# Performance work log

Hardware: AMD Instinct MI355X
Metric: run time of the kernel (lower is better)

## Reference

```python
import jax, jax.numpy as jnp
import numpy as np

B, S, D = 2, 2048, 1024
H_Q, H_KV, DK, DV = 16, 8, 64, 64
R = H_Q // H_KV  # q heads per kv head (GQA)
THETA = 10000.0


def setup_inputs() -> dict:
    key = jax.random.key(0)
    ks = jax.random.split(key, 12)
    inv_freq = 1.0 / (THETA ** (jnp.arange(0, DK, 2, dtype=jnp.float32) / DK))  # [DK/2]
    angles = jnp.arange(S, dtype=jnp.float32)[:, None] * inv_freq[None, :]      # [S, DK/2]
    scale = 0.02
    return {
        "x": jax.random.normal(ks[0], (B, S, D), jnp.float32),
        "Wq": jax.random.normal(ks[1], (D, H_Q * DK), jnp.float32) * scale,
        "bq": jnp.zeros((H_Q * DK,), jnp.float32),
        "Wk": jax.random.normal(ks[2], (D, H_KV * DK), jnp.float32) * scale,
        "bk": jnp.zeros((H_KV * DK,), jnp.float32),
        "Wv": jax.random.normal(ks[3], (D, H_KV * DV), jnp.float32) * scale,
        "bv": jnp.zeros((H_KV * DV,), jnp.float32),
        "Wo": jax.random.normal(ks[4], (H_Q * DV, D), jnp.float32) * scale,
        "bo": jnp.zeros((D,), jnp.float32),
        "freqs_cos": jnp.cos(angles),
        "freqs_sin": jnp.sin(angles),
        "attention_mask": jax.random.bernoulli(ks[5], 0.9, (B, S)),  # True = real token
    }


def _rope(t, cos, sin):
    # t: [B, S, H, Dh]; cos/sin: [S, Dh/2]. Complex rotation on interleaved pairs.
    tp = t.reshape(*t.shape[:-1], -1, 2)
    x1, x2 = tp[..., 0], tp[..., 1]
    c = cos[None, :, None, :]
    s = sin[None, :, None, :]
    o1 = x1 * c - x2 * s
    o2 = x1 * s + x2 * c
    return jnp.stack([o1, o2], axis=-1).reshape(t.shape)


def reference(x, Wq, bq, Wk, bk, Wv, bv, Wo, bo, freqs_cos, freqs_sin, attention_mask):
    b, s, _ = x.shape
    q = (x @ Wq + bq).reshape(b, s, H_Q, DK)
    k = (x @ Wk + bk).reshape(b, s, H_KV, DK)
    v = (x @ Wv + bv).reshape(b, s, H_KV, DV)
    q = _rope(q, freqs_cos, freqs_sin)
    k = _rope(k, freqs_cos, freqs_sin)
    q = q.transpose(0, 2, 1, 3)                      # [B, Hq, S, DK]
    k = jnp.repeat(k.transpose(0, 2, 1, 3), R, axis=1)  # GQA expand -> [B, Hq, S, DK]
    v = jnp.repeat(v.transpose(0, 2, 1, 3), R, axis=1)  # [B, Hq, S, DV]
    causal = jnp.tril(jnp.ones((s, s), dtype=bool))
    # Module does logical_or(padding, causal) -- replicated faithfully.
    mask = jnp.logical_or(attention_mask[:, None, None, :], causal[None, None])
    scale = 1.0 / jnp.sqrt(jnp.float32(DK))
    scores = jnp.einsum('bhqd,bhkd->bhqk', q, k) * scale
    scores = jnp.where(mask, scores, -jnp.inf)
    attn = jax.nn.softmax(scores, axis=-1)
    out = jnp.einsum('bhqk,bhkd->bhqd', attn, v)
    out = out.transpose(0, 2, 1, 3).reshape(b, s, H_Q * DV)
    return out @ Wo + bo
```

## Files before the change

kernel.cpp:

```cpp
#include <hip/hip_runtime.h>
#include <hip/hip_bf16.h>
#include <math.h>

typedef __attribute__((ext_vector_type(8))) short bf16x8;
typedef __attribute__((ext_vector_type(4))) float f32x4;

#define OFF_XB  0ull
#define OFF_WT  (8ull<<20)
#define OFF_WO  (12ull<<20)
#define OFF_QB  (14ull<<20)
#define OFF_KB  (22ull<<20)
#define OFF_VT  (26ull<<20)
#define OFF_AO  (30ull<<20)
#define OFF_MB  (38ull<<20)

#define QSCALE 0.18033688056680276f

__device__ inline unsigned pack_bf162(float a, float b) {
    __hip_bfloat162 t = __float22bfloat162_rn(make_float2(a, b));
    return *(unsigned*)&t;
}

__device__ inline float exp2_fast(float x) {
    float r;
    asm("v_exp_f32 %0, %1" : "=v"(r) : "v"(x));
    return r;
}

__device__ inline void gload16(const void* g, void* l) {
    __builtin_amdgcn_global_load_lds(
        (const __attribute__((address_space(1))) void*)g,
        (__attribute__((address_space(3))) void*)l, 16, 0, 0);
}

__launch_bounds__(256)
__global__ void prep_kernel(const float* __restrict__ x,
                            const float* __restrict__ Wq, const float* __restrict__ Wk,
                            const float* __restrict__ Wv, const float* __restrict__ Wo,
                            const void* __restrict__ mraw,
                            __hip_bfloat16* __restrict__ XB,
                            __hip_bfloat16* __restrict__ WT,
                            __hip_bfloat16* __restrict__ WoT,
                            float* __restrict__ mbias) {
    __shared__ float T[32][33];
    __shared__ int bad01, badf;
    const int tid = threadIdx.x;
    const int bid = blockIdx.x;
    if (bid < 1024) {
        const int base = bid * 4096;
#pragma unroll
        for (int i = 0; i < 4; ++i) {
            const int e = base + (i * 256 + tid) * 4;
            const float4 v = *(const float4*)&x[e];
            uint2 pk;
            pk.x = pack_bf162(v.x, v.y);
            pk.y = pack_bf162(v.z, v.w);
            *(uint2*)&XB[e] = pk;
        }
    } else if (bid < 4096) {
        const float* src; int ldn, nbase; __hip_bfloat16* dst; int n0, k0;
        if (bid < 3072) {
            const int tb = bid - 1024;
            const int kt = tb >> 6, nt = tb & 63;
            n0 = nt * 32; k0 = kt * 32; dst = WT;
            if (n0 < 1024)      { src = Wq; ldn = 1024; nbase = n0; }
            else if (n0 < 1536) { src = Wk; ldn = 512;  nbase = n0 - 1024; }
            else                { src = Wv; ldn = 512;  nbase = n0 - 1536; }
        } else {
            const int tb = bid - 3072;
            const int kt = tb >> 5, nt = tb & 31;
            n0 = nt * 32; k0 = kt * 32; dst = WoT;
            src = Wo; ldn = 1024; nbase = n0;
        }
        const int c = tid & 31, r0 = tid >> 5;
#pragma unroll
        for (int i = 0; i < 4; ++i)
            T[r0 + 8 * i][c] = src[(size_t)(k0 + r0 + 8 * i) * ldn + nbase + c];
        __syncthreads();
#pragma unroll
        for (int i = 0; i < 4; ++i) {
            const int nn = r0 + 8 * i;
            dst[(size_t)(n0 + nn) * 1024 + k0 + c] = __float2bfloat16(T[c][nn]);
        }
    } else {
        if (tid == 0) { bad01 = 0; badf = 0; }
        __syncthreads();
        const unsigned* w = (const unsigned*)mraw;
#pragma unroll
        for (int i = 0; i < 4; ++i) {
            const unsigned v = w[tid * 4 + i];
            if (v > 1u) atomicAdd(&bad01, 1);
            if (v != 0u && v != 0x3F800000u) atomicAdd(&badf, 1);
        }
        __syncthreads();
        const int fmt = (bad01 == 0) ? 0 : ((badf == 0) ? 1 : 2);
        for (int i = tid; i < 4096; i += 256) {
            bool on;
            if (fmt == 2) on = (((const unsigned char*)mraw)[i] != 0);
            else          on = (w[i] != 0u);
            mbias[i] = on ? 0.f : -1e30f;
        }
    }
}

#define QSTAGE(SEL, K0_) do {                                                    \
    _Pragma("unroll") for (int rnd_ = 0; rnd_ < 4; ++rnd_) {                     \
        const int off_ = rnd_ * 4096 + wid * 1024 + lane * 16;                   \
        const int row_ = off_ >> 7;                                              \
        const int ch_  = ((off_ >> 4) & 7) ^ (row_ & 7);                         \
        gload16((const char*)Ag + ((size_t)(n0 + row_) * 1024 + (K0_) + ch_ * 8) * 2, \
                Asm + (SEL) * 16384 + rnd_ * 4096 + wid * 1024);                 \
        gload16((const char*)Bg + ((size_t)(m0 + row_) * 1024 + (K0_) + ch_ * 8) * 2, \
                Bsm + (SEL) * 16384 + rnd_ * 4096 + wid * 1024);                 \
    }                                                                            \
} while (0)

__launch_bounds__(256)
__global__ void qkv_mfma_kernel(const __hip_bfloat16* __restrict__ XB,
                                const __hip_bfloat16* __restrict__ WT,
                                const float* __restrict__ bq, const float* __restrict__ bk,
                                const float* __restrict__ bv,
                                const float* __restrict__ fc, const float* __restrict__ fs,
                                __hip_bfloat16* __restrict__ QB,
                                __hip_bfloat16* __restrict__ KB,
                                __hip_bfloat16* __restrict__ VT) {
    __shared__ __attribute__((aligned(16))) char Asm[32768];
    __shared__ __attribute__((aligned(16))) char Bsm[32768];
    const int tid = threadIdx.x;
    const int lane = tid & 63, wid = tid >> 6;
    const int c = lane & 15, g = lane >> 4;
    const int n0 = blockIdx.x * 128, m0 = blockIdx.y * 128;
    const int wn = (wid >> 1) * 64, wm = (wid & 1) * 64;
    const __hip_bfloat16* Ag = WT;
    const __hip_bfloat16* Bg = XB;

    f32x4 acc[4][4];
#pragma unroll
    for (int ni = 0; ni < 4; ++ni)
#pragma unroll
        for (int mj = 0; mj < 4; ++mj) acc[ni][mj] = f32x4{0.f, 0.f, 0.f, 0.f};

    QSTAGE(0, 0);
    int cur = 0;
    for (int kt = 0; kt < 16; ++kt) {
        const int k0 = kt * 64;
        if (kt < 15) {
            QSTAGE(cur ^ 1, k0 + 64);
            asm volatile("s_waitcnt vmcnt(8)" ::: "memory");
        } else {
            asm volatile("s_waitcnt vmcnt(0)" ::: "memory");
        }
        __builtin_amdgcn_sched_barrier(0);
        __builtin_amdgcn_s_barrier();
        __builtin_amdgcn_sched_barrier(0);

        const char* Ac = Asm + cur * 16384;
        const char* Bc = Bsm + cur * 16384;
#pragma unroll
        for (int ks = 0; ks < 2; ++ks) {
            bf16x8 af[4], bfr[4];
#pragma unroll
            for (int t = 0; t < 4; ++t) {
                const int sl = ((g + 4 * ks) ^ (c & 7)) << 4;
                af[t]  = *(const bf16x8*)(Ac + (wn + 16 * t + c) * 128 + sl);
                bfr[t] = *(const bf16x8*)(Bc + (wm + 16 * t + c) * 128 + sl);
            }
#pragma unroll
            for (int ni = 0; ni < 4; ++ni)
#pragma unroll
                for (int mj = 0; mj < 4; ++mj)
                    acc[ni][mj] = __builtin_amdgcn_mfma_f32_16x16x32_bf16(
                        af[ni], bfr[mj], acc[ni][mj], 0, 0, 0);
        }
        __builtin_amdgcn_sched_barrier(0);
        __builtin_amdgcn_s_barrier();
        __builtin_amdgcn_sched_barrier(0);
        cur ^= 1;
    }

#pragma unroll
    for (int ni = 0; ni < 4; ++ni) {
        const int nb = n0 + wn + 16 * ni + 4 * g;
        const float* bias; int nloc;
        if (nb < 1024)      { bias = bq; nloc = nb; }
        else if (nb < 1536) { bias = bk; nloc = nb - 1024; }
        else                { bias = bv; nloc = nb - 1536; }
        const float4 b4 = *(const float4*)&bias[nloc];
        const int h = nloc >> 6, dk = nb & 63;
#pragma unroll
        for (int mj = 0; mj < 4; ++mj) {
            const int tok = m0 + wm + 16 * mj + c;
            const int bb = tok >> 11, sp = tok & 2047;
            float v0 = acc[ni][mj][0] + b4.x;
            float v1 = acc[ni][mj][1] + b4.y;
            float v2 = acc[ni][mj][2] + b4.z;
            float v3 = acc[ni][mj][3] + b4.w;
            if (nb < 1536) {
                const int p = sp * 32 + (dk >> 1);
                const float c0 = fc[p], s0 = fs[p];
                const float c1 = fc[p + 1], s1 = fs[p + 1];
                float o0 = v0 * c0 - v1 * s0, o1 = v0 * s0 + v1 * c0;
                float o2 = v2 * c1 - v3 * s1, o3 = v2 * s1 + v3 * c1;
                uint2 pk;
                if (nb < 1024) {
                    o0 *= QSCALE; o1 *= QSCALE; o2 *= QSCALE; o3 *= QSCALE;
                    pk.x = pack_bf162(o0, o1); pk.y = pack_bf162(o2, o3);
                    *(uint2*)&QB[(size_t)((bb * 16 + h) * 2048 + sp) * 64 + dk] = pk;
                } else {
                    pk.x = pack_bf162(o0, o1); pk.y = pack_bf162(o2, o3);
                    *(uint2*)&KB[(size_t)((bb * 8 + h) * 2048 + sp) * 64 + dk] = pk;
                }
            } else {
                const size_t vb = (size_t)((bb * 8 + h) * 64 + dk) * 2048 + sp;
                VT[vb]          = __float2bfloat16(v0);
                VT[vb + 2048]   = __float2bfloat16(v1);
                VT[vb + 4096]   = __float2bfloat16(v2);
                VT[vb + 6144]   = __float2bfloat16(v3);
            }
        }
    }
}

__launch_bounds__(256)
__global__ void out_mfma_kernel(const __hip_bfloat16* __restrict__ AOB,
                                const __hip_bfloat16* __restrict__ WoT,
                                const float* __restrict__ bo,
                                float* __restrict__ out) {
    __shared__ __attribute__((aligned(16))) char Asm[32768];
    __shared__ __attribute__((aligned(16))) char Bsm[32768];
    const int tid = threadIdx.x;
    const int lane = tid & 63, wid = tid >> 6;
    const int c = lane & 15, g = lane >> 4;
    const int n0 = blockIdx.x * 128, m0 = blockIdx.y * 128;
    const int wn = (wid >> 1) * 64, wm = (wid & 1) * 64;
    const __hip_bfloat16* Ag = WoT;
    const __hip_bfloat16* Bg = AOB;

    f32x4 acc[4][4];
#pragma unroll
    for (int ni = 0; ni < 4; ++ni)
#pragma unroll
        for (int mj = 0; mj < 4; ++mj) acc[ni][mj] = f32x4{0.f, 0.f, 0.f, 0.f};

    QSTAGE(0, 0);
    int cur = 0;
    for (int kt = 0; kt < 16; ++kt) {
        const int k0 = kt * 64;
        if (kt < 15) {
            QSTAGE(cur ^ 1, k0 + 64);
            asm volatile("s_waitcnt vmcnt(8)" ::: "memory");
        } else {
            asm volatile("s_waitcnt vmcnt(0)" ::: "memory");
        }
        __builtin_amdgcn_sched_barrier(0);
        __builtin_amdgcn_s_barrier();
        __builtin_amdgcn_sched_barrier(0);

        const char* Ac = Asm + cur * 16384;
        const char* Bc = Bsm + cur * 16384;
#pragma unroll
        for (int ks = 0; ks < 2; ++ks) {
            bf16x8 af[4], bfr[4];
#pragma unroll
            for (int t = 0; t < 4; ++t) {
                const int sl = ((g + 4 * ks) ^ (c & 7)) << 4;
                af[t]  = *(const bf16x8*)(Ac + (wn + 16 * t + c) * 128 + sl);
                bfr[t] = *(const bf16x8*)(Bc + (wm + 16 * t + c) * 128 + sl);
            }
#pragma unroll
            for (int ni = 0; ni < 4; ++ni)
#pragma unroll
                for (int mj = 0; mj < 4; ++mj)
                    acc[ni][mj] = __builtin_amdgcn_mfma_f32_16x16x32_bf16(
                        af[ni], bfr[mj], acc[ni][mj], 0, 0, 0);
        }
        __builtin_amdgcn_sched_barrier(0);
        __builtin_amdgcn_s_barrier();
        __builtin_amdgcn_sched_barrier(0);
        cur ^= 1;
    }
#pragma unroll
    for (int ni = 0; ni < 4; ++ni) {
        const int nb = n0 + wn + 16 * ni + 4 * g;
        const float4 b4 = *(const float4*)&bo[nb];
#pragma unroll
        for (int mj = 0; mj < 4; ++mj) {
            const int tok = m0 + wm + 16 * mj + c;
            const f32x4 a = acc[ni][mj];
            const float4 st = make_float4(a[0] + b4.x, a[1] + b4.y,
                                          a[2] + b4.z, a[3] + b4.w);
            *(float4*)&out[(size_t)tok * 1024 + nb] = st;
        }
    }
}


#define STAGE(BUFSEL, K0_) do {                                                  \
    _Pragma("unroll") for (int rnd_ = 0; rnd_ < 2; ++rnd_) {                     \
        const int off_ = rnd_ * 4096 + tid * 16;                                 \
        const int row_ = off_ >> 7;                                              \
        const int ch_  = ((off_ >> 4) & 7) ^ (row_ & 7);                         \
        gload16(Kh + (size_t)((K0_) + row_) * 64 + ch_ * 8,                      \
                Ksm + (BUFSEL) * 8192 + rnd_ * 4096 + wid * 1024);               \
        gload16(Vh + (size_t)row_ * 2048 + (K0_) + ch_ * 8,                      \
                Vsm + (BUFSEL) * 8192 + rnd_ * 4096 + wid * 1024);               \
    }                                                                            \
} while (0)

__launch_bounds__(256)
__global__ void attn_kernel(const __hip_bfloat16* __restrict__ QB,
                            const __hip_bfloat16* __restrict__ KB,
                            const __hip_bfloat16* __restrict__ VT,
                            const float* __restrict__ maskb,
                            __hip_bfloat16* __restrict__ AOB) {
    __shared__ __attribute__((aligned(16))) char Ksm[16384];
    __shared__ __attribute__((aligned(16))) char Vsm[16384];
    __shared__ char P_lds[4][4096];

    const int tid  = threadIdx.x;
    const int lane = tid & 63, wid = tid >> 6;
    const int c = lane & 15, g = lane >> 4;

    const int bid = blockIdx.x;
    const int o_  = (bid & 7) * 64 + (bid >> 3);
    const int qx = o_ & 15, h = (o_ >> 4) & 15, b = o_ >> 8;
    const int qb = qx * 128 + wid * 32;

    const __hip_bfloat16* Qh = QB + (size_t)(b * 16 + h)       * 2048 * 64;
    const __hip_bfloat16* Kh = KB + (size_t)(b * 8 + (h >> 1)) * 2048 * 64;
    const __hip_bfloat16* Vh = VT + (size_t)(b * 8 + (h >> 1)) * 64 * 2048;
    const float* mb = maskb + b * 2048;

    STAGE(0, 0);

    bf16x8 bq[2][2];
#pragma unroll
    for (int rt = 0; rt < 2; ++rt)
#pragma unroll
        for (int ks = 0; ks < 2; ++ks)
            bq[rt][ks] = *(const bf16x8*)&Qh[(size_t)(qb + 16 * rt + c) * 64
                                             + 32 * ks + 8 * g];
    __syncthreads();

    const short oneb = (short)0x3F80;
    const bf16x8 ones = {oneb, oneb, oneb, oneb, oneb, oneb, oneb, oneb};

    f32x4 o[2][4];
    f32x4 lacc[2];
#pragma unroll
    for (int rt = 0; rt < 2; ++rt) {
        lacc[rt] = f32x4{0.f, 0.f, 0.f, 0.f};
#pragma unroll
        for (int mt = 0; mt < 4; ++mt) o[rt][mt] = f32x4{0.f, 0.f, 0.f, 0.f};
    }
    float m_[2] = {-INFINITY, -INFINITY};

    char* Pw = &P_lds[wid][0];
    const int swz = (c & 7) << 4;

    int cur = 0;
    for (int kt = 0; kt < 32; ++kt) {
        const int k0 = kt * 64;
        if (kt < 31) {
            STAGE(cur ^ 1, k0 + 64);
            asm volatile("s_waitcnt vmcnt(4)" ::: "memory");
        } else {
            asm volatile("s_waitcnt vmcnt(0)" ::: "memory");
        }
        __builtin_amdgcn_sched_barrier(0);
        __builtin_amdgcn_s_barrier();
        __builtin_amdgcn_sched_barrier(0);

        const char* Kc = Ksm + cur * 8192;
        const char* Vc = Vsm + cur * 8192;

        bf16x8 ak[4][2];
#pragma unroll
        for (int mt = 0; mt < 4; ++mt)
#pragma unroll
            for (int ks = 0; ks < 2; ++ks)
                ak[mt][ks] = *(const bf16x8*)(Kc + (16 * mt + c) * 128
                                              + (((g + 4 * ks) ^ (c & 7)) << 4));

        const bool needb = (k0 + 63 > qb);
        float4 biasv[4];
        if (needb) {
#pragma unroll
            for (int mt = 0; mt < 4; ++mt)
                biasv[mt] = *(const float4*)&mb[k0 + 16 * mt + 4 * g];
        }

        __builtin_amdgcn_s_setprio(1);
        f32x4 st[2][4];
#pragma unroll
        for (int rt = 0; rt < 2; ++rt)
#pragma unroll
            for (int mt = 0; mt < 4; ++mt) {
                f32x4 z = f32x4{0.f, 0.f, 0.f, 0.f};
                z = __builtin_amdgcn_mfma_f32_16x16x32_bf16(ak[mt][0], bq[rt][0], z, 0, 0, 0);
                z = __builtin_amdgcn_mfma_f32_16x16x32_bf16(ak[mt][1], bq[rt][1], z, 0, 0, 0);
                st[rt][mt] = z;
            }
        __builtin_amdgcn_s_setprio(0);

        bf16x8 av[4][2];
#pragma unroll
        for (int mt = 0; mt < 4; ++mt)
#pragma unroll
            for (int ks = 0; ks < 2; ++ks)
                av[mt][ks] = *(const bf16x8*)(Vc + (16 * mt + c) * 128
                                              + (((g + 4 * ks) ^ (c & 7)) << 4));

#pragma unroll
        for (int rt = 0; rt < 2; ++rt) {
            const int qw = qb + 16 * rt;
            float pmax = -INFINITY;
            if (k0 + 63 <= qw) {
#pragma unroll
                for (int mt = 0; mt < 4; ++mt)
#pragma unroll
                    for (int r = 0; r < 4; ++r)
                        pmax = fmaxf(pmax, st[rt][mt][r]);
            } else if (k0 > qw + 15) {
#pragma unroll
                for (int mt = 0; mt < 4; ++mt) {
                    st[rt][mt][0] += biasv[mt].x; st[rt][mt][1] += biasv[mt].y;
                    st[rt][mt][2] += biasv[mt].z; st[rt][mt][3] += biasv[mt].w;
#pragma unroll
                    for (int r = 0; r < 4; ++r)
                        pmax = fmaxf(pmax, st[rt][mt][r]);
                }
            } else {
                const int qg = qw + c;
#pragma unroll
                for (int mt = 0; mt < 4; ++mt) {
                    const float bvr[4] = {biasv[mt].x, biasv[mt].y,
                                          biasv[mt].z, biasv[mt].w};
#pragma unroll
                    for (int r = 0; r < 4; ++r) {
                        const int kg = k0 + 16 * mt + 4 * g + r;
                        st[rt][mt][r] += (kg <= qg) ? 0.f : bvr[r];
                        pmax = fmaxf(pmax, st[rt][mt][r]);
                    }
                }
            }
            pmax = fmaxf(pmax, __shfl_xor(pmax, 16));
            pmax = fmaxf(pmax, __shfl_xor(pmax, 32));
            if (!__all(pmax <= m_[rt] + 11.5f)) {
                const float mn = fmaxf(m_[rt], pmax);
                const float alpha = exp2_fast(m_[rt] - mn);
                m_[rt] = mn;
                lacc[rt][0] *= alpha;
#pragma unroll
                for (int mt = 0; mt < 4; ++mt) o[rt][mt] *= alpha;
            }
#pragma unroll
            for (int mt = 0; mt < 4; ++mt)
#pragma unroll
                for (int r = 0; r < 4; ++r)
                    st[rt][mt][r] = exp2_fast(st[rt][mt][r] - m_[rt]);

            char* Pr = Pw + rt * 2048 + c * 128;
#pragma unroll
            for (int mt = 0; mt < 4; ++mt) {
                const unsigned w0 = pack_bf162(st[rt][mt][0], st[rt][mt][1]);
                const unsigned w1 = pack_bf162(st[rt][mt][2], st[rt][mt][3]);
                *(unsigned long long*)(Pr + ((32 * mt + 8 * g) ^ swz)) =
                    (unsigned long long)w0 | ((unsigned long long)w1 << 32);
            }
        }

#pragma unroll
        for (int rt = 0; rt < 2; ++rt) {
            const char* Pr = Pw + rt * 2048 + c * 128;
            const bf16x8 pb0 = *(const bf16x8*)(Pr + ((16 * g) ^ swz));
            const bf16x8 pb1 = *(const bf16x8*)(Pr + ((64 + 16 * g) ^ swz));
            __builtin_amdgcn_s_setprio(1);
#pragma unroll
            for (int mt = 0; mt < 4; ++mt) {
                o[rt][mt] = __builtin_amdgcn_mfma_f32_16x16x32_bf16(av[mt][0], pb0, o[rt][mt], 0, 0, 0);
                o[rt][mt] = __builtin_amdgcn_mfma_f32_16x16x32_bf16(av[mt][1], pb1, o[rt][mt], 0, 0, 0);
            }
            lacc[rt] = __builtin_amdgcn_mfma_f32_16x16x32_bf16(ones, pb0, lacc[rt], 0, 0, 0);
            lacc[rt] = __builtin_amdgcn_mfma_f32_16x16x32_bf16(ones, pb1, lacc[rt], 0, 0, 0);
            __builtin_amdgcn_s_setprio(0);
        }

        __builtin_amdgcn_sched_barrier(0);
        __builtin_amdgcn_s_barrier();
        __builtin_amdgcn_sched_barrier(0);
        cur ^= 1;
    }

#pragma unroll
    for (int rt = 0; rt < 2; ++rt) {
        const float inv = 1.f / lacc[rt][0];
        const size_t tok = (size_t)(b * 2048 + qb + 16 * rt + c);
#pragma unroll
        for (int mt = 0; mt < 4; ++mt) {
            uint2 pk;
            pk.x = pack_bf162(o[rt][mt][0] * inv, o[rt][mt][1] * inv);
            pk.y = pack_bf162(o[rt][mt][2] * inv, o[rt][mt][3] * inv);
            *(uint2*)&AOB[tok * 1024 + h * 64 + 16 * mt + 4 * g] = pk;
        }
    }
}

extern "C" void kernel_launch(void* const* d_in, const int* in_sizes, int n_in,
                              void* d_out, int out_size, void* d_ws, size_t ws_size,
                              hipStream_t stream) {
    const float* x  = (const float*)d_in[0];
    const float* Wq = (const float*)d_in[1];
    const float* bq = (const float*)d_in[2];
    const float* Wk = (const float*)d_in[3];
    const float* bk = (const float*)d_in[4];
    const float* Wv = (const float*)d_in[5];
    const float* bv = (const float*)d_in[6];
    const float* Wo = (const float*)d_in[7];
    const float* bo = (const float*)d_in[8];
    const float* fc = (const float*)d_in[9];
    const float* fs = (const float*)d_in[10];
    const void*  am = d_in[11];

    char* ws = (char*)d_ws;
    __hip_bfloat16* XB  = (__hip_bfloat16*)(ws + OFF_XB);
    __hip_bfloat16* WT  = (__hip_bfloat16*)(ws + OFF_WT);
    __hip_bfloat16* WoT = (__hip_bfloat16*)(ws + OFF_WO);
    __hip_bfloat16* QB  = (__hip_bfloat16*)(ws + OFF_QB);
    __hip_bfloat16* KB  = (__hip_bfloat16*)(ws + OFF_KB);
    __hip_bfloat16* VT  = (__hip_bfloat16*)(ws + OFF_VT);
    __hip_bfloat16* AOB = (__hip_bfloat16*)(ws + OFF_AO);
    float* mbias = (float*)(ws + OFF_MB);
    float* out   = (float*)d_out;

    hipLaunchKernelGGL(prep_kernel, dim3(4097), dim3(256), 0, stream,
                       x, Wq, Wk, Wv, Wo, am, XB, WT, WoT, mbias);
    hipLaunchKernelGGL(qkv_mfma_kernel, dim3(16, 32), dim3(256), 0, stream,
                       XB, WT, bq, bk, bv, fc, fs, QB, KB, VT);
    hipLaunchKernelGGL(attn_kernel, dim3(512), dim3(256), 0, stream,
                       QB, KB, VT, mbias, AOB);
    hipLaunchKernelGGL(out_mfma_kernel, dim3(8, 32), dim3(256), 0, stream,
                       AOB, WoT, bo, out);
}
```

Measured before the change: 139.4 us.

## Triple-buffer K/V tiles with one barrier per iteration and stage mask bias in LDS

Moves the attention inner loop from double to triple buffering of K/V tiles in shared memory, prefetching two tiles ahead and issuing the next load right after the single per-iteration barrier, so the trailing barrier can be dropped. The key-padding bias row is copied into LDS once up front instead of being read from global memory every tile. The row-max reduction is restructured into a tree of fmaxf calls to shorten the dependency chain. Shared-memory use grows by about 24 KB per block, which may reduce occupancy, and the vmcnt(4) wait count now has to match the two tiles in flight.

```diff
diff --git a/kernel.cpp b/kernel.cpp
--- a/kernel.cpp
+++ b/kernel.cpp
@@ -295,15 +295,17 @@
 }
 
 
-#define STAGE(BUFSEL, K0_) do {                                                  \
+#define STAGE3(T) do {                                                           \
+    const int buf_ = (T) % 3;                                                    \
+    const int tk0_ = (T) * 64;                                                   \
     _Pragma("unroll") for (int rnd_ = 0; rnd_ < 2; ++rnd_) {                     \
         const int off_ = rnd_ * 4096 + tid * 16;                                 \
         const int row_ = off_ >> 7;                                              \
         const int ch_  = ((off_ >> 4) & 7) ^ (row_ & 7);                         \
-        gload16(Kh + (size_t)((K0_) + row_) * 64 + ch_ * 8,                      \
-                Ksm + (BUFSEL) * 8192 + rnd_ * 4096 + wid * 1024);               \
-        gload16(Vh + (size_t)row_ * 2048 + (K0_) + ch_ * 8,                      \
-                Vsm + (BUFSEL) * 8192 + rnd_ * 4096 + wid * 1024);               \
+        gload16(Kh + (size_t)(tk0_ + row_) * 64 + ch_ * 8,                       \
+                Ksm + buf_ * 8192 + rnd_ * 4096 + wid * 1024);                   \
+        gload16(Vh + (size_t)row_ * 2048 + tk0_ + ch_ * 8,                       \
+                Vsm + buf_ * 8192 + rnd_ * 4096 + wid * 1024);                   \
     }                                                                            \
 } while (0)
 
@@ -313,9 +315,10 @@
                             const __hip_bfloat16* __restrict__ VT,
                             const float* __restrict__ maskb,
                             __hip_bfloat16* __restrict__ AOB) {
-    __shared__ __attribute__((aligned(16))) char Ksm[16384];
-    __shared__ __attribute__((aligned(16))) char Vsm[16384];
+    __shared__ __attribute__((aligned(16))) char Ksm[24576];
+    __shared__ __attribute__((aligned(16))) char Vsm[24576];
     __shared__ char P_lds[4][4096];
+    __shared__ float bias_sm[2048];
 
     const int tid  = threadIdx.x;
     const int lane = tid & 63, wid = tid >> 6;
@@ -331,8 +334,6 @@
     const __hip_bfloat16* Vh = VT + (size_t)(b * 8 + (h >> 1)) * 64 * 2048;
     const float* mb = maskb + b * 2048;
 
-    STAGE(0, 0);
-
     bf16x8 bq[2][2];
 #pragma unroll
     for (int rt = 0; rt < 2; ++rt)
@@ -340,6 +341,10 @@
         for (int ks = 0; ks < 2; ++ks)
             bq[rt][ks] = *(const bf16x8*)&Qh[(size_t)(qb + 16 * rt + c) * 64
                                              + 32 * ks + 8 * g];
+    for (int i = tid; i < 512; i += 256)
+        *(float4*)&bias_sm[4 * i] = *(const float4*)&mb[4 * i];
+    STAGE3(0);
+    STAGE3(1);
     __syncthreads();
 
     const short oneb = (short)0x3F80;
@@ -358,11 +363,9 @@
     char* Pw = &P_lds[wid][0];
     const int swz = (c & 7) << 4;
 
-    int cur = 0;
     for (int kt = 0; kt < 32; ++kt) {
         const int k0 = kt * 64;
         if (kt < 31) {
-            STAGE(cur ^ 1, k0 + 64);
             asm volatile("s_waitcnt vmcnt(4)" ::: "memory");
         } else {
             asm volatile("s_waitcnt vmcnt(0)" ::: "memory");
@@ -370,9 +373,10 @@
         __builtin_amdgcn_sched_barrier(0);
         __builtin_amdgcn_s_barrier();
         __builtin_amdgcn_sched_barrier(0);
-
-        const char* Kc = Ksm + cur * 8192;
-        const char* Vc = Vsm + cur * 8192;
+        if (kt < 30) STAGE3(kt + 2);
+
+        const char* Kc = Ksm + (kt % 3) * 8192;
+        const char* Vc = Vsm + (kt % 3) * 8192;
 
         bf16x8 ak[4][2];
 #pragma unroll
@@ -387,7 +391,7 @@
         if (needb) {
 #pragma unroll
             for (int mt = 0; mt < 4; ++mt)
-                biasv[mt] = *(const float4*)&mb[k0 + 16 * mt + 4 * g];
+                biasv[mt] = *(const float4*)&bias_sm[k0 + 16 * mt + 4 * g];
         }
 
         __builtin_amdgcn_s_setprio(1);
@@ -414,21 +418,12 @@
 #pragma unroll
         for (int rt = 0; rt < 2; ++rt) {
             const int qw = qb + 16 * rt;
-            float pmax = -INFINITY;
             if (k0 + 63 <= qw) {
-#pragma unroll
-                for (int mt = 0; mt < 4; ++mt)
-#pragma unroll
-                    for (int r = 0; r < 4; ++r)
-                        pmax = fmaxf(pmax, st[rt][mt][r]);
             } else if (k0 > qw + 15) {
 #pragma unroll
                 for (int mt = 0; mt < 4; ++mt) {
                     st[rt][mt][0] += biasv[mt].x; st[rt][mt][1] += biasv[mt].y;
                     st[rt][mt][2] += biasv[mt].z; st[rt][mt][3] += biasv[mt].w;
-#pragma unroll
-                    for (int r = 0; r < 4; ++r)
-                        pmax = fmaxf(pmax, st[rt][mt][r]);
                 }
             } else {
                 const int qg = qw + c;
@@ -440,10 +435,15 @@
                     for (int r = 0; r < 4; ++r) {
                         const int kg = k0 + 16 * mt + 4 * g + r;
                         st[rt][mt][r] += (kg <= qg) ? 0.f : bvr[r];
-                        pmax = fmaxf(pmax, st[rt][mt][r]);
                     }
                 }
             }
+            float mx[4];
+#pragma unroll
+            for (int mt = 0; mt < 4; ++mt)
+                mx[mt] = fmaxf(fmaxf(st[rt][mt][0], st[rt][mt][1]),
+                               fmaxf(st[rt][mt][2], st[rt][mt][3]));
+            float pmax = fmaxf(fmaxf(mx[0], mx[1]), fmaxf(mx[2], mx[3]));
             pmax = fmaxf(pmax, __shfl_xor(pmax, 16));
             pmax = fmaxf(pmax, __shfl_xor(pmax, 32));
             if (!__all(pmax <= m_[rt] + 11.5f)) {
@@ -485,11 +485,6 @@
             lacc[rt] = __builtin_amdgcn_mfma_f32_16x16x32_bf16(ones, pb1, lacc[rt], 0, 0, 0);
             __builtin_amdgcn_s_setprio(0);
         }
-
-        __builtin_amdgcn_sched_barrier(0);
-        __builtin_amdgcn_s_barrier();
-        __builtin_amdgcn_sched_barrier(0);
-        cur ^= 1;
     }
 
 #pragma unroll
```

Measured after the change: 145.5 us. 1.04x slower.
